# Optimization experiments

Measured on AMD Instinct MI355X. Metric: run time of the kernel, lower is better.

The kernel has to match this reference:

```python
import jax, jax.numpy as jnp
import numpy as np

DIM_M = 512
NEG_INF = -1e30


def setup_inputs() -> dict:
    key = jax.random.key(0)
    k1, k2, k3, k4, k5, k6, k7 = jax.random.split(key, 7)
    B, Lc, Lq, d = 16, 1024, 512, DIM_M
    C = jax.random.normal(k1, (B, Lc, d), dtype=jnp.float32)
    Q = jax.random.normal(k2, (B, Lq, d), dtype=jnp.float32)
    cmask = jax.random.randint(k3, (B, Lc), 0, 2).astype(jnp.float32)
    qmask = jax.random.randint(k4, (B, Lq), 0, 2).astype(jnp.float32)
    lim = np.sqrt(1.0 / d)
    w = jax.random.uniform(k5, (3 * d,), minval=-lim, maxval=lim, dtype=jnp.float32)
    # out_linear: Linear(4d -> d), torch default init
    bound = np.sqrt(1.0 / (4 * d))
    out_w = jax.random.uniform(k6, (d, 4 * d), minval=-bound, maxval=bound, dtype=jnp.float32)
    out_b = jax.random.uniform(k7, (d,), minval=-bound, maxval=bound, dtype=jnp.float32)
    return {"C": C, "Q": Q, "cmask": cmask, "qmask": qmask, "w": w, "out_w": out_w, "out_b": out_b}


def _mask_logits(t, m):
    return t * m + (1.0 - m) * NEG_INF


def reference(C, Q, cmask, qmask, w, out_w, out_b):
    d = C.shape[-1]
    w1, w2, w3 = w[:d], w[d:2 * d], w[2 * d:]
    # Decomposed trilinear similarity (same math as cat([Ct,Qt,Ct*Qt]) @ w):
    # S[b,i,j] = C[b,i]@w1 + Q[b,j]@w2 + (C[b,i]*w3) @ Q[b,j]
    S = (C @ w1)[:, :, None] + (Q @ w2)[:, None, :] \
        + jnp.einsum('bid,bjd->bij', C * w3, Q)  # [B, Lc, Lq]
    qm = qmask[:, None, :]  # [B, 1, Lq]
    cm = cmask[:, :, None]  # [B, Lc, 1]
    S1 = jax.nn.softmax(_mask_logits(S, qm), axis=2)  # over Lq
    S2 = jax.nn.softmax(_mask_logits(S, cm), axis=1)  # over Lc
    A = jnp.einsum('bij,bjd->bid', S1, Q)  # [B, Lc, d]
    # bmm(bmm(S1, S2^T), C) == S1 @ (S2^T @ C) by associativity (cheaper)
    S2TC = jnp.einsum('bij,bid->bjd', S2, C)  # [B, Lq, d]
    Bm = jnp.einsum('bij,bjd->bid', S1, S2TC)  # [B, Lc, d]
    out = jnp.concatenate([C, A, C * A, C * Bm], axis=2)  # [B, Lc, 4d]
    # dropout inactive (inference); out_linear
    return out @ out_w.T + out_b
```

## Files before the change

kernel.cpp:

```cpp
#include <hip/hip_runtime.h>
#include <hip/hip_bf16.h>


#define NB 16
#define LC 1024
#define LQ 512
#define DM 512
#define D4 2048
#define NEGINF (-1e30f)

typedef __bf16 v8bf __attribute__((ext_vector_type(8)));
typedef __bf16 v4bf __attribute__((ext_vector_type(4)));
typedef float  v4f  __attribute__((ext_vector_type(4)));

#define MFMA16 __builtin_amdgcn_mfma_f32_16x16x32_bf16

#define GLOAD16(gp, lp) __builtin_amdgcn_global_load_lds( \
    (const __attribute__((address_space(1))) void*)(gp), \
    (__attribute__((address_space(3))) void*)(lp), 16, 0, 0)

#define GEMM_PROLOG \
  __shared__ __bf16 Al[2][128 * 64], Bl[2][64 * 64]; \
  int bx = blockIdx.x, by = blockIdx.y, bz = blockIdx.z; \
  xcd_remap(bx, by, bz); \
  const int b = bz, i0 = by * 128, n0 = bx * 64; \
  const int t = threadIdx.x, lane = t & 63, wave = t >> 6; \
  const int wm = wave >> 1, wn = wave & 1, quad = lane >> 4, col = lane & 15; \
  const int srA = wave * 32 + (lane >> 3); \
  const int srB = wave * 16 + (lane >> 3); \
  const int swz = ((lane & 7) ^ (lane >> 3)) * 8; \
  const int q80 = ((quad ^ (col & 7)) * 8); \
  const int q81 = (((4 + quad) ^ (col & 7)) * 8); \
  v4f acc[4][2]; \
  _Pragma("unroll") for (int x = 0; x < 4; ++x) \
  _Pragma("unroll") for (int y = 0; y < 2; ++y) \
  _Pragma("unroll") for (int r = 0; r < 4; ++r) acc[x][y][r] = 0.f;

#define GEMM_STAGE(buf, Aptr, Bptr, LDGA, LDGB, k0) \
  do { \
    _Pragma("unroll") for (int u = 0; u < 4; ++u) \
      GLOAD16((Aptr) + (size_t)(u * 8) * (LDGA) + (k0), &Al[buf][(wave * 32 + u * 8) * 64]); \
    _Pragma("unroll") for (int u = 0; u < 2; ++u) \
      GLOAD16((Bptr) + (size_t)(u * 8) * (LDGB) + (k0), &Bl[buf][(wave * 16 + u * 8) * 64]); \
  } while (0)

#define GEMM_COMPUTE(buf) \
  do { \
    v8bf af_[4], bf_[2]; \
    _Pragma("unroll") for (int x = 0; x < 4; ++x) \
      af_[x] = *(const v8bf*)&Al[buf][(wm * 64 + x * 16 + col) * 64 + q80]; \
    _Pragma("unroll") for (int y = 0; y < 2; ++y) \
      bf_[y] = *(const v8bf*)&Bl[buf][(wn * 32 + y * 16 + col) * 64 + q80]; \
    _Pragma("unroll") for (int x = 0; x < 4; ++x) \
    _Pragma("unroll") for (int y = 0; y < 2; ++y) \
      acc[x][y] = MFMA16(af_[x], bf_[y], acc[x][y], 0, 0, 0); \
    _Pragma("unroll") for (int x = 0; x < 4; ++x) \
      af_[x] = *(const v8bf*)&Al[buf][(wm * 64 + x * 16 + col) * 64 + q81]; \
    _Pragma("unroll") for (int y = 0; y < 2; ++y) \
      bf_[y] = *(const v8bf*)&Bl[buf][(wn * 32 + y * 16 + col) * 64 + q81]; \
    _Pragma("unroll") for (int x = 0; x < 4; ++x) \
    _Pragma("unroll") for (int y = 0; y < 2; ++y) \
      acc[x][y] = MFMA16(af_[x], bf_[y], acc[x][y], 0, 0, 0); \
  } while (0)

#define GEMM_SYNC() \
  do { asm volatile("s_waitcnt vmcnt(0)" ::: "memory"); \
       __builtin_amdgcn_s_barrier(); } while (0)

#define GEMM_KLOOP(Arow, Brow, LDGA, LDGB, KEXT) \
  { GEMM_STAGE(0, Arow, Brow, LDGA, LDGB, 0); \
    GEMM_SYNC(); \
    int cur_ = 0; \
    for (int k0 = 0; k0 < (KEXT); k0 += 64) { \
      const int kn_ = k0 + 64; \
      if (kn_ < (KEXT)) GEMM_STAGE(cur_ ^ 1, Arow, Brow, LDGA, LDGB, kn_); \
      GEMM_COMPUTE(cur_); \
      GEMM_SYNC(); \
      cur_ ^= 1; \
    } }

__device__ __forceinline__ void xcd_remap(int& bx, int& by, int& bz) {
  const int gx = gridDim.x, gy = gridDim.y, gz = gridDim.z;
  int flat = bx + gx * (by + gy * bz);
  int per = (gx * gy * gz) >> 3;
  int nw = (flat & 7) * per + (flat >> 3);
  bx = nw % gx;
  int r = nw / gx;
  by = r % gy;
  bz = r / gy;
}

__global__ void k_rowdots(const float* __restrict__ C, const float* __restrict__ Q,
                          const float* __restrict__ w,
                          float* __restrict__ cw1, float* __restrict__ qw2,
                          __bf16* __restrict__ Cbf, __bf16* __restrict__ Qw3) {
  const int wid = threadIdx.x >> 6, lane = threadIdx.x & 63;
  const int row = blockIdx.x * 4 + wid;
  const bool isC = row < NB * LC;
  const int lr = isC ? row : row - NB * LC;
  const float* src = (isC ? C : Q) + (size_t)lr * DM;
  const float* wv  = isC ? w : (w + DM);
  const float* w3  = w + 2 * DM;
  __bf16* dst = (isC ? Cbf : Qw3) + (size_t)lr * DM;
  float v = 0.f;
#pragma unroll
  for (int s = 0; s < 2; ++s) {
    const int k = lane * 4 + s * 256;
    float4 f = *(const float4*)(src + k);
    float4 g = *(const float4*)(wv + k);
    v += f.x * g.x + f.y * g.y + f.z * g.z + f.w * g.w;
    v4bf h;
    if (isC) {
      h[0] = (__bf16)f.x; h[1] = (__bf16)f.y; h[2] = (__bf16)f.z; h[3] = (__bf16)f.w;
    } else {
      float4 s3 = *(const float4*)(w3 + k);
      h[0] = (__bf16)(f.x * s3.x); h[1] = (__bf16)(f.y * s3.y);
      h[2] = (__bf16)(f.z * s3.z); h[3] = (__bf16)(f.w * s3.w);
    }
    *(v4bf*)(dst + k) = h;
  }
#pragma unroll
  for (int off = 32; off; off >>= 1) v += __shfl_down(v, off, 64);
  if (lane == 0) {
    if (isC) cw1[row] = v;
    else     qw2[lr] = v;
  }
}

__device__ __forceinline__ void transpose_tile_f32(const float* __restrict__ in,
                                                   __bf16* __restrict__ outT,
                                                   int R, int Cd, int tbx, int tby, int tb) {
  __shared__ __bf16 tile[64][66];
  const int r0 = tby * 64, c0 = tbx * 64;
  const int tr = threadIdx.x >> 6, tc = threadIdx.x & 63;
  const float* inb = in + (size_t)tb * R * Cd;
  __bf16* outb = outT + (size_t)tb * Cd * R;
  for (int r = tr; r < 64; r += 4)
    tile[r][tc] = (__bf16)inb[(size_t)(r0 + r) * Cd + c0 + tc];
  __syncthreads();
  for (int c = tr; c < 64; c += 4)
    outb[(size_t)(c0 + c) * R + r0 + tc] = tile[tc][c];
}

__device__ __forceinline__ void transpose_tile_bf(const __bf16* __restrict__ in,
                                                  __bf16* __restrict__ outT,
                                                  int R, int Cd, int tbx, int tby, int tb) {
  __shared__ __bf16 tile[64][66];
  const int r0 = tby * 64, c0 = tbx * 64;
  const int tr = threadIdx.x >> 6, tc = threadIdx.x & 63;
  const __bf16* inb = in + (size_t)tb * R * Cd;
  __bf16* outb = outT + (size_t)tb * Cd * R;
  for (int r = tr; r < 64; r += 4)
    tile[r][tc] = inb[(size_t)(r0 + r) * Cd + c0 + tc];
  __syncthreads();
  for (int c = tr; c < 64; c += 4)
    outb[(size_t)(c0 + c) * R + r0 + tc] = tile[tc][c];
}

__global__ void k_prep(const float* __restrict__ C, const __bf16* __restrict__ Cbf,
                       const float* __restrict__ Q, const float* __restrict__ OW,
                       __bf16* __restrict__ CT, __bf16* __restrict__ QT,
                       __bf16* __restrict__ OWb, int use_cbf) {
  const int id = blockIdx.x;
  if (id < 2048) {
    if (use_cbf) transpose_tile_bf(Cbf, CT, LC, DM, id & 7, (id >> 3) & 15, id >> 7);
    else         transpose_tile_f32(C,  CT, LC, DM, id & 7, (id >> 3) & 15, id >> 7);
  } else if (id < 3072) {
    const int id2 = id - 2048;
    transpose_tile_f32(Q, QT, LQ, DM, id2 & 7, (id2 >> 3) & 7, id2 >> 6);
  } else {
    const size_t i = ((size_t)(id - 3072) * 256 + threadIdx.x) * 4;
    float4 f = *(const float4*)(OW + i);
    v4bf h; h[0] = (__bf16)f.x; h[1] = (__bf16)f.y; h[2] = (__bf16)f.z; h[3] = (__bf16)f.w;
    *(v4bf*)(OWb + i) = h;
  }
}

__global__ void k_cvt2b(const float* __restrict__ Cf, const float* __restrict__ OW,
                        __bf16* __restrict__ Cb3, __bf16* __restrict__ OWb) {
  const size_t NC = (size_t)NB * LC * DM;
  size_t i = ((size_t)blockIdx.x * 256 + threadIdx.x) * 4;
  if (i < NC) {
    float4 f = *(const float4*)(Cf + i);
    v4bf h; h[0] = (__bf16)f.x; h[1] = (__bf16)f.y; h[2] = (__bf16)f.z; h[3] = (__bf16)f.w;
    *(v4bf*)(Cb3 + i) = h;
  } else {
    size_t j = i - NC;
    float4 f = *(const float4*)(OW + j);
    v4bf h; h[0] = (__bf16)f.x; h[1] = (__bf16)f.y; h[2] = (__bf16)f.z; h[3] = (__bf16)f.w;
    *(v4bf*)(OWb + j) = h;
  }
}

__global__ __launch_bounds__(256) void k_mfma_S(
    const __bf16* __restrict__ Cbf, const __bf16* __restrict__ Qw3,
    const float* __restrict__ cw1, const float* __restrict__ qw2,
    float* __restrict__ S) {
  GEMM_PROLOG
  const __bf16* Arow = Cbf + (size_t)b * LC * DM + (size_t)(i0 + srA) * DM + swz;
  const __bf16* Brow = Qw3 + (size_t)b * LQ * DM + (size_t)(n0 + srB) * DM + swz;
  GEMM_KLOOP(Arow, Brow, DM, DM, DM)
  float* Sb = S + (size_t)b * LC * LQ;
#pragma unroll
  for (int x = 0; x < 4; ++x) {
    const int mB = i0 + wm * 64 + x * 16 + quad * 4;
    float cv[4];
#pragma unroll
    for (int r = 0; r < 4; ++r) cv[r] = cw1[b * LC + mB + r];
#pragma unroll
    for (int y = 0; y < 2; ++y) {
      const int j = n0 + wn * 32 + y * 16 + col;
      const float qv = qw2[b * LQ + j];
#pragma unroll
      for (int r = 0; r < 4; ++r)
        Sb[(size_t)(mB + r) * LQ + j] = acc[x][y][r] + cv[r] + qv;
    }
  }
}

__global__ __launch_bounds__(1024) void k_softstat(
    const float* __restrict__ S, const float* __restrict__ qmask,
    const float* __restrict__ cmask, __bf16* __restrict__ S1,
    float2* __restrict__ pstat) {
  __shared__ float2 cst[16][LQ];
  const int b = blockIdx.y, ic = blockIdx.x;
  const int tid = threadIdx.x, wv = tid >> 6, lane = tid & 63;
  const float* qm  = qmask + b * LQ;
  const float* cm  = cmask + b * LC + ic * 64;
  const float* Sb  = S  + ((size_t)b * LC + ic * 64) * LQ;
  __bf16*      S1b = S1 + ((size_t)b * LC + ic * 64) * LQ;
  float colm[8], cols[8];
#pragma unroll
  for (int tt = 0; tt < 8; ++tt) { colm[tt] = -3e38f; cols[tt] = 0.f; }
  for (int it = 0; it < 4; ++it) {
    const int r = wv * 4 + it;
    const float cmv = cm[r];
    const float* Srow = Sb + (size_t)r * LQ;
    float sv[8], l1[8];
    float m = -3e38f;
#pragma unroll
    for (int tt = 0; tt < 8; ++tt) {
      int j = lane + 64 * tt;
      sv[tt] = Srow[j];
      float qv = qm[j];
      l1[tt] = qv * sv[tt] + (1.f - qv) * NEGINF;
      m = fmaxf(m, l1[tt]);
    }
#pragma unroll
    for (int off = 32; off; off >>= 1) m = fmaxf(m, __shfl_xor(m, off, 64));
    float e[8], s = 0.f;
#pragma unroll
    for (int tt = 0; tt < 8; ++tt) { e[tt] = __expf(l1[tt] - m); s += e[tt]; }
#pragma unroll
    for (int off = 32; off; off >>= 1) s += __shfl_xor(s, off, 64);
    const float inv = 1.f / s;
#pragma unroll
    for (int tt = 0; tt < 8; ++tt)
      S1b[(size_t)r * LQ + lane + 64 * tt] = (__bf16)(e[tt] * inv);
    if (cmv != 0.f) {
#pragma unroll
      for (int tt = 0; tt < 8; ++tt) {
        float l2 = sv[tt];
        if (l2 > colm[tt]) { cols[tt] *= __expf(colm[tt] - l2); colm[tt] = l2; }
        cols[tt] += __expf(l2 - colm[tt]);
      }
    }
  }
#pragma unroll
  for (int tt = 0; tt < 8; ++tt) cst[wv][lane + 64 * tt] = make_float2(colm[tt], cols[tt]);
  __syncthreads();
  if (tid < LQ) {
    float M = -3e38f, Sd = 0.f;
#pragma unroll
    for (int k = 0; k < 16; ++k) {
      float2 p = cst[k][tid];
      float nM = fmaxf(M, p.x);
      Sd = Sd * __expf(M - nM) + p.y * __expf(p.x - nM);
      M = nM;
    }
    pstat[((size_t)(b * 16 + ic) * LQ) + tid] = make_float2(M, Sd);
  }
}

__global__ void k_colwrite(const float* __restrict__ S, const float* __restrict__ cmask,
                           const float2* __restrict__ pstat, __bf16* __restrict__ S2T) {
  __shared__ float Mf[64], If[64];
  __shared__ __bf16 tile[64][66];
  const int b = blockIdx.z, ic = blockIdx.y, j0 = blockIdx.x * 64;
  const int c = threadIdx.x & 63, ip = threadIdx.x >> 6;
  if (threadIdx.x < 64) {
    float M = -3e38f, Sd = 0.f;
#pragma unroll
    for (int k = 0; k < 16; ++k) {
      float2 p = pstat[((size_t)(b * 16 + k) * LQ) + j0 + threadIdx.x];
      float nM = fmaxf(M, p.x);
      Sd = Sd * __expf(M - nM) + p.y * __expf(p.x - nM);
      M = nM;
    }
    Mf[threadIdx.x] = M; If[threadIdx.x] = 1.f / Sd;
  }
  __syncthreads();
  const float M = Mf[c], inv = If[c];
  const float* Sb = S + ((size_t)b * LC + ic * 64) * LQ;
  const float* cm = cmask + b * LC + ic * 64;
  for (int r = ip; r < 64; r += 4) {
    if (cm[r] != 0.f)
      tile[r][c] = (__bf16)(__expf(Sb[(size_t)r * LQ + j0 + c] - M) * inv);
    else
      tile[r][c] = (__bf16)0.f;
  }
  __syncthreads();
  __bf16* S2Tb = S2T + ((size_t)b * LQ + j0) * LC + ic * 64;
  for (int jr = ip; jr < 64; jr += 4)
    S2Tb[(size_t)jr * LC + c] = tile[c][jr];
}

__global__ __launch_bounds__(256) void k_mfma_A(
    const __bf16* __restrict__ S1, const __bf16* __restrict__ QT,
    const float* __restrict__ Cf, __bf16* __restrict__ Aw, __bf16* __restrict__ CAw) {
  GEMM_PROLOG
  const __bf16* Arow = S1 + (size_t)b * LC * LQ + (size_t)(i0 + srA) * LQ + swz;
  const __bf16* Brow = QT + (size_t)b * DM * LQ + (size_t)(n0 + srB) * LQ + swz;
  GEMM_KLOOP(Arow, Brow, LQ, LQ, LQ)
  const float* Cb = Cf + (size_t)b * LC * DM;
  __bf16* Ab  = Aw  + (size_t)b * LC * DM;
  __bf16* CAb = CAw + (size_t)b * LC * DM;
#pragma unroll
  for (int x = 0; x < 4; ++x) {
    const int mB = i0 + wm * 64 + x * 16 + quad * 4;
#pragma unroll
    for (int y = 0; y < 2; ++y) {
      const int n = n0 + wn * 32 + y * 16 + col;
#pragma unroll
      for (int r = 0; r < 4; ++r) {
        const float av = acc[x][y][r];
        const float cv = Cb[(size_t)(mB + r) * DM + n];
        Ab[(size_t)(mB + r) * DM + n]  = (__bf16)av;
        CAb[(size_t)(mB + r) * DM + n] = (__bf16)(av * cv);
      }
    }
  }
}

__global__ __launch_bounds__(256) void k_mfma_T(
    const __bf16* __restrict__ S2T, const __bf16* __restrict__ CT, __bf16* __restrict__ S2TCT) {
  GEMM_PROLOG
  const int j0 = i0;
  const __bf16* Arow = S2T + (size_t)b * LQ * LC + (size_t)(j0 + srA) * LC + swz;
  const __bf16* Brow = CT  + (size_t)b * DM * LC + (size_t)(n0 + srB) * LC + swz;
  GEMM_KLOOP(Arow, Brow, LC, LC, LC)
#pragma unroll
  for (int x = 0; x < 4; ++x) {
    const int jB = j0 + wm * 64 + x * 16 + quad * 4;
#pragma unroll
    for (int y = 0; y < 2; ++y) {
      const int n = n0 + wn * 32 + y * 16 + col;
      v4bf h;
#pragma unroll
      for (int r = 0; r < 4; ++r) h[r] = (__bf16)acc[x][y][r];
      *(v4bf*)&S2TCT[((size_t)b * DM + n) * LQ + jB] = h;
    }
  }
}

__global__ __launch_bounds__(256) void k_mfma_Bm(
    const __bf16* __restrict__ S1, const __bf16* __restrict__ S2TCT,
    const float* __restrict__ Cf, __bf16* __restrict__ CBw) {
  GEMM_PROLOG
  const __bf16* Arow = S1    + (size_t)b * LC * LQ + (size_t)(i0 + srA) * LQ + swz;
  const __bf16* Brow = S2TCT + (size_t)b * DM * LQ + (size_t)(n0 + srB) * LQ + swz;
  GEMM_KLOOP(Arow, Brow, LQ, LQ, LQ)
  const float* Cb = Cf + (size_t)b * LC * DM;
  __bf16* CBb = CBw + (size_t)b * LC * DM;
#pragma unroll
  for (int x = 0; x < 4; ++x) {
    const int mB = i0 + wm * 64 + x * 16 + quad * 4;
#pragma unroll
    for (int y = 0; y < 2; ++y) {
      const int n = n0 + wn * 32 + y * 16 + col;
#pragma unroll
      for (int r = 0; r < 4; ++r) {
        const float cv = Cb[(size_t)(mB + r) * DM + n];
        CBb[(size_t)(mB + r) * DM + n] = (__bf16)(acc[x][y][r] * cv);
      }
    }
  }
}

__global__ __launch_bounds__(256) void k_mfma_out(
    const __bf16* __restrict__ Cb3, const __bf16* __restrict__ Aw,
    const __bf16* __restrict__ CAw, const __bf16* __restrict__ CBw,
    const __bf16* __restrict__ OWb, const float* __restrict__ ob,
    float* __restrict__ out) {
  GEMM_PROLOG
  const size_t rowoff = (size_t)b * LC * DM + (size_t)(i0 + srA) * DM + swz;
  const __bf16* As0 = Cb3 + rowoff;
  const __bf16* As1 = Aw  + rowoff;
  const __bf16* As2 = CAw + rowoff;
  const __bf16* As3 = CBw + rowoff;
  const __bf16* Brow0 = OWb + (size_t)(n0 + srB) * D4 + swz;
  GEMM_STAGE(0, As0, Brow0, DM, D4, 0);
  GEMM_SYNC();
  int cur_ = 0;
#pragma unroll
  for (int seg = 0; seg < 4; ++seg) {
    const __bf16* Arow  = (seg == 0) ? As0 : (seg == 1) ? As1 : (seg == 2) ? As2 : As3;
    const __bf16* Anext = (seg == 0) ? As1 : (seg == 1) ? As2 : As3;
    const __bf16* Brow  = Brow0 + seg * DM;
    const __bf16* Bnext = Brow0 + (seg < 3 ? seg + 1 : 3) * DM;
    for (int k0 = 0; k0 < DM; k0 += 64) {
      const int kn_ = k0 + 64;
      if (kn_ < DM)      GEMM_STAGE(cur_ ^ 1, Arow, Brow, DM, D4, kn_);
      else if (seg < 3)  GEMM_STAGE(cur_ ^ 1, Anext, Bnext, DM, D4, 0);
      GEMM_COMPUTE(cur_);
      GEMM_SYNC();
      cur_ ^= 1;
    }
  }
  float* outb = out + (size_t)b * LC * DM;
#pragma unroll
  for (int x = 0; x < 4; ++x) {
    const int mB = i0 + wm * 64 + x * 16 + quad * 4;
#pragma unroll
    for (int y = 0; y < 2; ++y) {
      const int n = n0 + wn * 32 + y * 16 + col;
      const float bv = ob[n];
#pragma unroll
      for (int r = 0; r < 4; ++r)
        outb[(size_t)(mB + r) * DM + n] = acc[x][y][r] + bv;
    }
  }
}

extern "C" void kernel_launch(void* const* d_in, const int* in_sizes, int n_in,
                              void* d_out, int out_size, void* d_ws, size_t ws_size,
                              hipStream_t stream) {
  const float* C     = (const float*)d_in[0];
  const float* Q     = (const float*)d_in[1];
  const float* cmask = (const float*)d_in[2];
  const float* qmask = (const float*)d_in[3];
  const float* w     = (const float*)d_in[4];
  const float* out_w = (const float*)d_in[5];
  const float* out_b = (const float*)d_in[6];
  float* out = (float*)d_out;

  char* base = (char*)d_ws;
  float*  cw1   = (float*)base;
  float*  qw2   = (float*)(base + 65536);
  char*   R     = base + 131072;
  float*  S     = (float*)R;
  __bf16* CT    = (__bf16*)R;
  __bf16* Aw    = (__bf16*)R;
  __bf16* QT    = (__bf16*)(R + (16u << 20));
  __bf16* CBw   = (__bf16*)(R + (16u << 20));
  __bf16* S1    = (__bf16*)(R + (32u << 20));
  __bf16* Qw3   = (__bf16*)(R + (48u << 20));
  __bf16* S2T   = (__bf16*)(R + (48u << 20));
  __bf16* CAw   = (__bf16*)(R + (48u << 20));
  float2* pstat = (float2*)(R + (64u << 20));
  __bf16* S2TCT = (__bf16*)(R + (64u << 20));
  (void)in_sizes; (void)n_in; (void)out_size;

  const size_t need_big = 131072 + (90ull << 20);
  const bool bigws = ws_size >= need_big;

  __bf16 *Cbf, *Cbf3, *OWbf;
  if (bigws) {
    Cbf  = (__bf16*)(R + (72u << 20));
    Cbf3 = Cbf;
    OWbf = (__bf16*)(R + (88u << 20));
  } else {
    Cbf  = (__bf16*)(R + (32u << 20));
    Cbf3 = (__bf16*)(R + (32u << 20));
    OWbf = (__bf16*)(R + (64u << 20));
  }

  k_rowdots<<<(NB * LC + NB * LQ) / 4, 256, 0, stream>>>(C, Q, w, cw1, qw2, Cbf, Qw3);
  k_mfma_S<<<dim3(LQ / 64, LC / 128, NB), 256, 0, stream>>>(Cbf, Qw3, cw1, qw2, S);
  k_softstat<<<dim3(LC / 64, NB), 1024, 0, stream>>>(S, qmask, cmask, S1, pstat);
  k_colwrite<<<dim3(LQ / 64, LC / 64, NB), 256, 0, stream>>>(S, cmask, pstat, S2T);
  k_prep<<<bigws ? 4096 : 3072, 256, 0, stream>>>(C, Cbf, Q, out_w, CT, QT, OWbf,
                                                  bigws ? 1 : 0);
  k_mfma_T<<<dim3(DM / 64, LQ / 128, NB), 256, 0, stream>>>(S2T, CT, S2TCT);
  k_mfma_A<<<dim3(DM / 64, LC / 128, NB), 256, 0, stream>>>(S1, QT, C, Aw, CAw);
  k_mfma_Bm<<<dim3(DM / 64, LC / 128, NB), 256, 0, stream>>>(S1, S2TCT, C, CBw);
  if (!bigws)
    k_cvt2b<<<(NB * LC * DM + DM * D4) / 1024, 256, 0, stream>>>(C, out_w, Cbf3, OWbf);
  k_mfma_out<<<dim3(DM / 64, LC / 128, NB), 256, 0, stream>>>(Cbf3, Aw, CAw, CBw, OWbf, out_b, out);
}
```

Before: 292.6 us.

## Retile output GEMM to 128x128 with three-stage K=32 load pipeline

The output projection GEMM now uses 128x128 tiles with K steps of 32 and a triple-buffered LDS pipeline. It waits with vmcnt(4), so one stage of global-to-LDS loads can stay in flight while the MFMAs run. The larger N tile doubles A-operand reuse and halves the number of blocks. The cost is more accumulator registers, a new swizzle pattern, and fewer blocks (512) to fill the CUs. The other GEMMs only have their macros renamed.

```diff
diff --git a/kernel.cpp b/kernel.cpp
--- a/kernel.cpp
+++ b/kernel.cpp
@@ -19,7 +19,18 @@
     (const __attribute__((address_space(1))) void*)(gp), \
     (__attribute__((address_space(3))) void*)(lp), 16, 0, 0)
 
-#define GEMM_PROLOG \
+__device__ __forceinline__ void xcd_remap(int& bx, int& by, int& bz) {
+  const int gx = gridDim.x, gy = gridDim.y, gz = gridDim.z;
+  int flat = bx + gx * (by + gy * bz);
+  int per = (gx * gy * gz) >> 3;
+  int nw = (flat & 7) * per + (flat >> 3);
+  bx = nw % gx;
+  int r = nw / gx;
+  by = r % gy;
+  bz = r / gy;
+}
+
+#define P_PROLOG \
   __shared__ __bf16 Al[2][128 * 64], Bl[2][64 * 64]; \
   int bx = blockIdx.x, by = blockIdx.y, bz = blockIdx.z; \
   xcd_remap(bx, by, bz); \
@@ -36,7 +47,7 @@
   _Pragma("unroll") for (int y = 0; y < 2; ++y) \
   _Pragma("unroll") for (int r = 0; r < 4; ++r) acc[x][y][r] = 0.f;
 
-#define GEMM_STAGE(buf, Aptr, Bptr, LDGA, LDGB, k0) \
+#define P_STAGE(buf, Aptr, Bptr, LDGA, LDGB, k0) \
   do { \
     _Pragma("unroll") for (int u = 0; u < 4; ++u) \
       GLOAD16((Aptr) + (size_t)(u * 8) * (LDGA) + (k0), &Al[buf][(wave * 32 + u * 8) * 64]); \
@@ -44,7 +55,7 @@
       GLOAD16((Bptr) + (size_t)(u * 8) * (LDGB) + (k0), &Bl[buf][(wave * 16 + u * 8) * 64]); \
   } while (0)
 
-#define GEMM_COMPUTE(buf) \
+#define P_COMPUTE(buf) \
   do { \
     v8bf af_[4], bf_[2]; \
     _Pragma("unroll") for (int x = 0; x < 4; ++x) \
@@ -63,32 +74,66 @@
       acc[x][y] = MFMA16(af_[x], bf_[y], acc[x][y], 0, 0, 0); \
   } while (0)
 
-#define GEMM_SYNC() \
+#define P_SYNC() \
   do { asm volatile("s_waitcnt vmcnt(0)" ::: "memory"); \
        __builtin_amdgcn_s_barrier(); } while (0)
 
-#define GEMM_KLOOP(Arow, Brow, LDGA, LDGB, KEXT) \
-  { GEMM_STAGE(0, Arow, Brow, LDGA, LDGB, 0); \
-    GEMM_SYNC(); \
+#define P_KLOOP(Arow, Brow, LDGA, LDGB, KEXT) \
+  { P_STAGE(0, Arow, Brow, LDGA, LDGB, 0); \
+    P_SYNC(); \
     int cur_ = 0; \
     for (int k0 = 0; k0 < (KEXT); k0 += 64) { \
       const int kn_ = k0 + 64; \
-      if (kn_ < (KEXT)) GEMM_STAGE(cur_ ^ 1, Arow, Brow, LDGA, LDGB, kn_); \
-      GEMM_COMPUTE(cur_); \
-      GEMM_SYNC(); \
+      if (kn_ < (KEXT)) P_STAGE(cur_ ^ 1, Arow, Brow, LDGA, LDGB, kn_); \
+      P_COMPUTE(cur_); \
+      P_SYNC(); \
       cur_ ^= 1; \
     } }
 
-__device__ __forceinline__ void xcd_remap(int& bx, int& by, int& bz) {
-  const int gx = gridDim.x, gy = gridDim.y, gz = gridDim.z;
-  int flat = bx + gx * (by + gy * bz);
-  int per = (gx * gy * gz) >> 3;
-  int nw = (flat & 7) * per + (flat >> 3);
-  bx = nw % gx;
-  int r = nw / gx;
-  by = r % gy;
-  bz = r / gy;
-}
+#define O_PROLOG \
+  __shared__ __bf16 Al[3][128 * 32], Bl[3][128 * 32]; \
+  int bx = blockIdx.x, by = blockIdx.y, bz = blockIdx.z; \
+  xcd_remap(bx, by, bz); \
+  const int b = bz, i0 = by * 128, n0 = bx * 128; \
+  const int t = threadIdx.x, lane = t & 63, wave = t >> 6; \
+  const int wm = wave >> 1, wn = wave & 1, quad = lane >> 4, col = lane & 15; \
+  const int sr32 = wave * 32 + (lane >> 2); \
+  const int swz = (((lane & 3) ^ ((lane >> 2) & 3) ^ ((lane >> 4) & 3)) * 8); \
+  const int rdx = ((quad ^ (col & 3) ^ ((col >> 2) & 3)) * 8); \
+  v4f acc[4][4]; \
+  _Pragma("unroll") for (int x = 0; x < 4; ++x) \
+  _Pragma("unroll") for (int y = 0; y < 4; ++y) \
+  _Pragma("unroll") for (int r = 0; r < 4; ++r) acc[x][y][r] = 0.f;
+
+#define O_STAGE(buf, Aptr, Bptr, LDGA, LDGB, k0) \
+  do { \
+    GLOAD16((Aptr) + (k0),                       &Al[buf][(wave * 32) * 32]); \
+    GLOAD16((Aptr) + (size_t)16 * (LDGA) + (k0), &Al[buf][(wave * 32 + 16) * 32]); \
+    GLOAD16((Bptr) + (k0),                       &Bl[buf][(wave * 32) * 32]); \
+    GLOAD16((Bptr) + (size_t)16 * (LDGB) + (k0), &Bl[buf][(wave * 32 + 16) * 32]); \
+  } while (0)
+
+#define O_COMPUTE(buf) \
+  do { \
+    v8bf af_[4], bf_[4]; \
+    _Pragma("unroll") for (int x = 0; x < 4; ++x) \
+      af_[x] = *(const v8bf*)&Al[buf][(wm * 64 + x * 16 + col) * 32 + rdx]; \
+    _Pragma("unroll") for (int y = 0; y < 4; ++y) \
+      bf_[y] = *(const v8bf*)&Bl[buf][(wn * 64 + y * 16 + col) * 32 + rdx]; \
+    _Pragma("unroll") for (int x = 0; x < 4; ++x) \
+    _Pragma("unroll") for (int y = 0; y < 4; ++y) \
+      acc[x][y] = MFMA16(af_[x], bf_[y], acc[x][y], 0, 0, 0); \
+  } while (0)
+
+#define O_SYNC4() \
+  do { asm volatile("s_waitcnt vmcnt(4)" ::: "memory"); \
+       __builtin_amdgcn_s_barrier(); } while (0)
+#define O_SYNC0() \
+  do { asm volatile("s_waitcnt vmcnt(0)" ::: "memory"); \
+       __builtin_amdgcn_s_barrier(); } while (0)
+
+#define O_ROT() do { cur_ = (cur_ == 2) ? 0 : cur_ + 1; \
+                     nx2_ = (nx2_ == 2) ? 0 : nx2_ + 1; } while (0)
 
 __global__ void k_rowdots(const float* __restrict__ C, const float* __restrict__ Q,
                           const float* __restrict__ w,
@@ -196,10 +241,10 @@
     const __bf16* __restrict__ Cbf, const __bf16* __restrict__ Qw3,
     const float* __restrict__ cw1, const float* __restrict__ qw2,
     float* __restrict__ S) {
-  GEMM_PROLOG
+  P_PROLOG
   const __bf16* Arow = Cbf + (size_t)b * LC * DM + (size_t)(i0 + srA) * DM + swz;
   const __bf16* Brow = Qw3 + (size_t)b * LQ * DM + (size_t)(n0 + srB) * DM + swz;
-  GEMM_KLOOP(Arow, Brow, DM, DM, DM)
+  P_KLOOP(Arow, Brow, DM, DM, DM)
   float* Sb = S + (size_t)b * LC * LQ;
 #pragma unroll
   for (int x = 0; x < 4; ++x) {
@@ -318,10 +363,10 @@
 __global__ __launch_bounds__(256) void k_mfma_A(
     const __bf16* __restrict__ S1, const __bf16* __restrict__ QT,
     const float* __restrict__ Cf, __bf16* __restrict__ Aw, __bf16* __restrict__ CAw) {
-  GEMM_PROLOG
+  P_PROLOG
   const __bf16* Arow = S1 + (size_t)b * LC * LQ + (size_t)(i0 + srA) * LQ + swz;
   const __bf16* Brow = QT + (size_t)b * DM * LQ + (size_t)(n0 + srB) * LQ + swz;
-  GEMM_KLOOP(Arow, Brow, LQ, LQ, LQ)
+  P_KLOOP(Arow, Brow, LQ, LQ, LQ)
   const float* Cb = Cf + (size_t)b * LC * DM;
   __bf16* Ab  = Aw  + (size_t)b * LC * DM;
   __bf16* CAb = CAw + (size_t)b * LC * DM;
@@ -344,11 +389,11 @@
 
 __global__ __launch_bounds__(256) void k_mfma_T(
     const __bf16* __restrict__ S2T, const __bf16* __restrict__ CT, __bf16* __restrict__ S2TCT) {
-  GEMM_PROLOG
+  P_PROLOG
   const int j0 = i0;
   const __bf16* Arow = S2T + (size_t)b * LQ * LC + (size_t)(j0 + srA) * LC + swz;
   const __bf16* Brow = CT  + (size_t)b * DM * LC + (size_t)(n0 + srB) * LC + swz;
-  GEMM_KLOOP(Arow, Brow, LC, LC, LC)
+  P_KLOOP(Arow, Brow, LC, LC, LC)
 #pragma unroll
   for (int x = 0; x < 4; ++x) {
     const int jB = j0 + wm * 64 + x * 16 + quad * 4;
@@ -366,10 +411,10 @@
 __global__ __launch_bounds__(256) void k_mfma_Bm(
     const __bf16* __restrict__ S1, const __bf16* __restrict__ S2TCT,
     const float* __restrict__ Cf, __bf16* __restrict__ CBw) {
-  GEMM_PROLOG
+  P_PROLOG
   const __bf16* Arow = S1    + (size_t)b * LC * LQ + (size_t)(i0 + srA) * LQ + swz;
   const __bf16* Brow = S2TCT + (size_t)b * DM * LQ + (size_t)(n0 + srB) * LQ + swz;
-  GEMM_KLOOP(Arow, Brow, LQ, LQ, LQ)
+  P_KLOOP(Arow, Brow, LQ, LQ, LQ)
   const float* Cb = Cf + (size_t)b * LC * DM;
   __bf16* CBb = CBw + (size_t)b * LC * DM;
 #pragma unroll
@@ -392,29 +437,40 @@
     const __bf16* __restrict__ CAw, const __bf16* __restrict__ CBw,
     const __bf16* __restrict__ OWb, const float* __restrict__ ob,
     float* __restrict__ out) {
-  GEMM_PROLOG
-  const size_t rowoff = (size_t)b * LC * DM + (size_t)(i0 + srA) * DM + swz;
-  const __bf16* As0 = Cb3 + rowoff;
-  const __bf16* As1 = Aw  + rowoff;
-  const __bf16* As2 = CAw + rowoff;
-  const __bf16* As3 = CBw + rowoff;
-  const __bf16* Brow0 = OWb + (size_t)(n0 + srB) * D4 + swz;
-  GEMM_STAGE(0, As0, Brow0, DM, D4, 0);
-  GEMM_SYNC();
-  int cur_ = 0;
+  O_PROLOG
+  const size_t rowoff = (size_t)b * LC * DM + (size_t)(i0 + sr32) * DM + swz;
+  const __bf16* Aseg[4] = {Cb3 + rowoff, Aw + rowoff, CAw + rowoff, CBw + rowoff};
+  const __bf16* Brow0 = OWb + (size_t)(n0 + sr32) * D4 + swz;
+  O_STAGE(0, Aseg[0], Brow0, DM, D4, 0);
+  O_STAGE(1, Aseg[0], Brow0, DM, D4, 32);
+  O_SYNC4();
+  int cur_ = 0, nx2_ = 2;
 #pragma unroll
   for (int seg = 0; seg < 4; ++seg) {
-    const __bf16* Arow  = (seg == 0) ? As0 : (seg == 1) ? As1 : (seg == 2) ? As2 : As3;
-    const __bf16* Anext = (seg == 0) ? As1 : (seg == 1) ? As2 : As3;
-    const __bf16* Brow  = Brow0 + seg * DM;
-    const __bf16* Bnext = Brow0 + (seg < 3 ? seg + 1 : 3) * DM;
-    for (int k0 = 0; k0 < DM; k0 += 64) {
-      const int kn_ = k0 + 64;
-      if (kn_ < DM)      GEMM_STAGE(cur_ ^ 1, Arow, Brow, DM, D4, kn_);
-      else if (seg < 3)  GEMM_STAGE(cur_ ^ 1, Anext, Bnext, DM, D4, 0);
-      GEMM_COMPUTE(cur_);
-      GEMM_SYNC();
-      cur_ ^= 1;
+    const __bf16* Ac = Aseg[seg];
+    const __bf16* An = Aseg[seg < 3 ? seg + 1 : 3];
+    const __bf16* Bc = Brow0 + seg * DM;
+    const __bf16* Bn = Brow0 + (seg < 3 ? seg + 1 : 3) * DM;
+    for (int j = 0; j < 14; ++j) {
+      O_STAGE(nx2_, Ac, Bc, DM, D4, (j + 2) * 32);
+      O_COMPUTE(cur_);
+      O_SYNC4();
+      O_ROT();
+    }
+    if (seg < 3) {
+      O_STAGE(nx2_, An, Bn, DM, D4, 0);
+      O_COMPUTE(cur_);
+      O_SYNC4();
+      O_ROT();
+      O_STAGE(nx2_, An, Bn, DM, D4, 32);
+      O_COMPUTE(cur_);
+      O_SYNC4();
+      O_ROT();
+    } else {
+      O_COMPUTE(cur_);
+      O_SYNC0();
+      O_ROT();
+      O_COMPUTE(cur_);
     }
   }
   float* outb = out + (size_t)b * LC * DM;
@@ -422,8 +478,8 @@
   for (int x = 0; x < 4; ++x) {
     const int mB = i0 + wm * 64 + x * 16 + quad * 4;
 #pragma unroll
-    for (int y = 0; y < 2; ++y) {
-      const int n = n0 + wn * 32 + y * 16 + col;
+    for (int y = 0; y < 4; ++y) {
+      const int n = n0 + wn * 64 + y * 16 + col;
       const float bv = ob[n];
 #pragma unroll
       for (int r = 0; r < 4; ++r)
@@ -486,5 +542,5 @@
   k_mfma_Bm<<<dim3(DM / 64, LC / 128, NB), 256, 0, stream>>>(S1, S2TCT, C, CBw);
   if (!bigws)
     k_cvt2b<<<(NB * LC * DM + DM * D4) / 1024, 256, 0, stream>>>(C, out_w, Cbf3, OWbf);
-  k_mfma_out<<<dim3(DM / 64, LC / 128, NB), 256, 0, stream>>>(Cbf3, Aw, CAw, CBw, OWbf, out_b, out);
-}
+  k_mfma_out<<<dim3(DM / 128, LC / 128, NB), 256, 0, stream>>>(Cbf3, Aw, CAw, CBw, OWbf, out_b, out);
+}
```

New measurement: 273.8 us. 6.4% less time.
